# Performance work log

Hardware: AMD Instinct MI355X
Metric: run time of the kernel (lower is better)

## Reference

```python
import jax, jax.numpy as jnp
import numpy as np

N_NODES = 100000
N_EDGES = 1600000
IN_CH = 128
HID = 128
N_GRAPHS = 256


def gcn_conv(x, W, b, src, dst, n_nodes):
    """PyG GCNConv: linear -> symmetric degree normalization with self-loops -> scatter-add -> bias."""
    h = x @ W  # [N, H]
    # degree (in-degree on target index) including the added self-loop
    deg = 1.0 + jax.ops.segment_sum(jnp.ones((dst.shape[0],), x.dtype), dst, num_segments=n_nodes)
    dis = deg ** -0.5  # deg >= 1, no inf guard needed
    coef = dis[src] * dis[dst]  # [E]
    agg = jax.ops.segment_sum(h[src] * coef[:, None], dst, num_segments=n_nodes)
    # self-loop contribution: h[i] * dis[i]^2 = h[i] / deg[i]
    agg = agg + h * (1.0 / deg)[:, None]
    return agg + b


def global_mean_pool(x, batch, n_graphs):
    sums = jax.ops.segment_sum(x, batch, num_segments=n_graphs)
    cnts = jax.ops.segment_sum(jnp.ones((x.shape[0],), x.dtype), batch, num_segments=n_graphs)
    return sums / jnp.maximum(cnts, 1.0)[:, None]


def setup_inputs() -> dict:
    key = jax.random.key(0)
    ks = jax.random.split(key, 8)
    x = jax.random.normal(ks[0], (N_NODES, IN_CH), dtype=jnp.float32)
    edge_index = jax.random.randint(ks[1], (2, N_EDGES), 0, N_NODES, dtype=jnp.int32)
    batch = jnp.sort(jax.random.randint(ks[2], (N_NODES,), 0, N_GRAPHS, dtype=jnp.int32))
    # glorot-ish init for weights
    s1 = (6.0 / (IN_CH + HID)) ** 0.5
    W1 = jax.random.uniform(ks[3], (IN_CH, HID), jnp.float32, -s1, s1)
    b1 = jnp.zeros((HID,), jnp.float32)
    s2 = (6.0 / (HID + HID)) ** 0.5
    W2 = jax.random.uniform(ks[4], (HID, HID), jnp.float32, -s2, s2)
    b2 = jnp.zeros((HID,), jnp.float32)
    s3 = (6.0 / (HID + 1)) ** 0.5
    Wfc = jax.random.uniform(ks[5], (HID, 1), jnp.float32, -s3, s3)
    bfc = jnp.zeros((1,), jnp.float32)
    return {"x": x, "edge_index": edge_index, "batch": batch,
            "W1": W1, "b1": b1, "W2": W2, "b2": b2, "Wfc": Wfc, "bfc": bfc}


def reference(x, edge_index, batch, W1, b1, W2, b2, Wfc, bfc):
    src, dst = edge_index[0], edge_index[1]
    h = jax.nn.relu(gcn_conv(x, W1, b1, src, dst, N_NODES))
    h = jax.nn.relu(gcn_conv(h, W2, b2, src, dst, N_NODES))
    g = global_mean_pool(h, batch, N_GRAPHS)  # [G, H]
    out = g @ Wfc + bfc  # [G, 1]
    return out.squeeze(-1)
```

## Files before the change

kernel.cpp:

```cpp
#include <hip/hip_runtime.h>
#include <hip/hip_bf16.h>

#define N_NODES 100000
#define N_EDGES 1600000
#define HID 128
#define N_GRAPHS 256

#define BSHIFT 9
#define BSIZE 512
#define NBUCK ((N_NODES + BSIZE - 1) / BSIZE)
#define BCAP 12288
#define EPB 8192
#define NBLK_A ((N_EDGES + EPB - 1) / EPB)
#define NCLS 16
#define ZOFF ((uint)N_NODES << 8)

typedef unsigned int uint;
typedef unsigned short ushort;
typedef short short8 __attribute__((ext_vector_type(8)));
typedef float f32x4 __attribute__((ext_vector_type(4)));

__device__ __forceinline__ ushort f2bf_hw(float f) {
    union { __hip_bfloat16 b; ushort u; } cv;
    cv.b = __float2bfloat16(f);
    return cv.u;
}
__device__ __forceinline__ uint4 pack8(const float* r) {
    uint4 o;
    o.x = (uint)f2bf_hw(r[0]) | ((uint)f2bf_hw(r[1]) << 16);
    o.y = (uint)f2bf_hw(r[2]) | ((uint)f2bf_hw(r[3]) << 16);
    o.z = (uint)f2bf_hw(r[4]) | ((uint)f2bf_hw(r[5]) << 16);
    o.w = (uint)f2bf_hw(r[6]) | ((uint)f2bf_hw(r[7]) << 16);
    return o;
}
__device__ __forceinline__ void accp(uint4 v, float2* a) {
    a[0].x += __uint_as_float(v.x << 16);
    a[0].y += __uint_as_float(v.x & 0xFFFF0000u);
    a[1].x += __uint_as_float(v.y << 16);
    a[1].y += __uint_as_float(v.y & 0xFFFF0000u);
    a[2].x += __uint_as_float(v.z << 16);
    a[2].y += __uint_as_float(v.z & 0xFFFF0000u);
    a[3].x += __uint_as_float(v.w << 16);
    a[3].y += __uint_as_float(v.w & 0xFFFF0000u);
}

union Frag16 {
    uint4 u;
    short8 s;
    ushort h[8];
};

__global__ void setup_kernel(int* __restrict__ bfill, int* __restrict__ clshist,
                             int* __restrict__ clsfill,
                             uint4* __restrict__ Azr, uint4* __restrict__ Bzr,
                             const float* __restrict__ W1, const float* __restrict__ W2,
                             uint4* __restrict__ WB1, uint4* __restrict__ WB2) {
    if (blockIdx.x == 0) {
        int t = threadIdx.x;
        if (t < NBUCK) bfill[t] = 0;
        if (t < NCLS) { clshist[t] = 0; clsfill[t] = 0; }
        if (t < 16) Azr[t] = (uint4){0, 0, 0, 0};
        else if (t < 32) Bzr[t - 16] = (uint4){0, 0, 0, 0};
        return;
    }
    int t = (blockIdx.x - 1) * 256 + threadIdx.x;
    const float* W = (t < 2048) ? W1 : W2;
    uint4* WB = (t < 2048) ? WB1 : WB2;
    int tt = t & 2047;
    int lane = tt & 63;
    int nt = (tt >> 6) & 7;
    int kt = tt >> 9;
    int kbase = kt * 32 + (lane >> 4) * 8;
    int col = nt * 16 + (lane & 15);
    float r[8];
#pragma unroll
    for (int j = 0; j < 8; j++) r[j] = W[(size_t)(kbase + j) * 128 + col];
    WB[tt] = pack8(r);
}

__global__ __launch_bounds__(256) void bucket_scatter_kernel(const int* __restrict__ src,
                                                             const int* __restrict__ dst,
                                                             int* __restrict__ bfill,
                                                             uint* __restrict__ bucketed) {
    __shared__ int h[NBUCK];
    __shared__ int rb[NBUCK];
    for (int t = threadIdx.x; t < NBUCK; t += 256) h[t] = 0;
    __syncthreads();
    int base = blockIdx.x * EPB;
#pragma unroll 4
    for (int it = 0; it < EPB / 256; ++it) {
        int e = base + it * 256 + threadIdx.x;
        if (e < N_EDGES) atomicAdd(&h[dst[e] >> BSHIFT], 1);
    }
    __syncthreads();
    for (int t = threadIdx.x; t < NBUCK; t += 256) {
        rb[t] = (h[t] ? atomicAdd(&bfill[t], h[t]) : 0) + t * BCAP;
        h[t] = 0;
    }
    __syncthreads();
#pragma unroll 4
    for (int it = 0; it < EPB / 256; ++it) {
        int e = base + it * 256 + threadIdx.x;
        if (e < N_EDGES) {
            int d = dst[e];
            int b = d >> BSHIFT;
            int pos = rb[b] + atomicAdd(&h[b], 1);
            bucketed[pos] = (uint)src[e] | ((uint)(d & (BSIZE - 1)) << 17);
        }
    }
}

__global__ __launch_bounds__(256) void bucket_csr_kernel(const uint* __restrict__ bucketed,
                                                         const int* __restrict__ bfill,
                                                         int* __restrict__ degi,
                                                         int* __restrict__ rowptr,
                                                         float* __restrict__ dis,
                                                         uint* __restrict__ csrb,
                                                         int* __restrict__ clshist) {
    int b = blockIdx.x;
    int beg = b * BCAP;
    int ne = bfill[b];
    __shared__ int cnt[BSIZE];
    __shared__ int fl[BSIZE];
    __shared__ int ex[BSIZE];
    __shared__ int ps[256];
    __shared__ int ch[NCLS];
    int t = threadIdx.x;
    cnt[t] = 0; cnt[t + 256] = 0;
    fl[t] = 0;  fl[t + 256] = 0;
    if (t < NCLS) ch[t] = 0;
    __syncthreads();
    for (int i = t; i < ne; i += 256) atomicAdd(&cnt[bucketed[beg + i] >> 17], 1);
    __syncthreads();
    int v0 = cnt[2 * t], v1 = cnt[2 * t + 1];
    int p0 = (v0 + 3) & ~3;
    int p1 = (v1 + 3) & ~3;
    int s = p0 + p1;
    ps[t] = s;
    __syncthreads();
    for (int off = 1; off < 256; off <<= 1) {
        int a = (t >= off) ? ps[t - off] : 0;
        __syncthreads();
        ps[t] += a;
        __syncthreads();
    }
    int e0 = ps[t] - s;
    ex[2 * t] = e0;
    ex[2 * t + 1] = e0 + p0;
    int g = b * BSIZE + 2 * t;
    if (g < N_NODES) {
        degi[g] = p0; rowptr[g] = beg + e0;
        dis[g] = rsqrtf(1.0f + (float)v0);
        atomicAdd(&ch[min(p0 >> 2, NCLS - 1)], 1);
    }
    if (g + 1 < N_NODES) {
        degi[g + 1] = p1; rowptr[g + 1] = beg + e0 + p0;
        dis[g + 1] = rsqrtf(1.0f + (float)v1);
        atomicAdd(&ch[min(p1 >> 2, NCLS - 1)], 1);
    }
    __syncthreads();
    if (t < NCLS && ch[t]) atomicAdd(&clshist[t], ch[t]);
    for (int i = t; i < ne; i += 256) {
        uint u = bucketed[beg + i];
        int dl = u >> 17;
        int p = ex[dl] + atomicAdd(&fl[dl], 1);
        csrb[beg + p] = (u & 0x1FFFFu) << 8;
    }
    __syncthreads();
    for (int p = v0; p < p0; ++p) csrb[beg + ex[2 * t] + p] = ZOFF;
    for (int p = v1; p < p1; ++p) csrb[beg + ex[2 * t + 1] + p] = ZOFF;
}

__global__ void clsbase_kernel(const int* __restrict__ clshist, int* __restrict__ clsbase) {
    if (threadIdx.x == 0) {
        int run = 0;
        for (int c = 0; c < NCLS; ++c) { clsbase[c] = run; run += clshist[c]; }
    }
}

__global__ __launch_bounds__(256) void perm_kernel(const int* __restrict__ degi,
                                                   const int* __restrict__ clsbase,
                                                   int* __restrict__ clsfill,
                                                   int* __restrict__ perm) {
    __shared__ int h[NCLS];
    __shared__ int rb[NCLS];
    int t = threadIdx.x;
    if (t < NCLS) h[t] = 0;
    __syncthreads();
    int n = blockIdx.x * 256 + t;
    int cls = 0, myloc = 0;
    if (n < N_NODES) {
        cls = min(degi[n] >> 2, NCLS - 1);
        myloc = atomicAdd(&h[cls], 1);
    }
    __syncthreads();
    if (t < NCLS) rb[t] = h[t] ? (clsbase[t] + atomicAdd(&clsfill[t], h[t])) : 0;
    __syncthreads();
    if (n < N_NODES) perm[rb[cls] + myloc] = n;
}

__global__ __launch_bounds__(256) void xprep_kernel(const float* __restrict__ x,
                                                    const float* __restrict__ dis,
                                                    uint4* __restrict__ Xp) {
    int t = blockIdx.x * 256 + threadIdx.x;
    if (t >= N_NODES * 16) return;
    int n = t >> 4, c16 = t & 15;
    const float* xr = x + (size_t)n * 128 + c16 * 8;
    float d = dis[n];
    float4 lo = *(const float4*)xr;
    float4 hi = *(const float4*)(xr + 4);
    float r[8] = {d * lo.x, d * lo.y, d * lo.z, d * lo.w,
                  d * hi.x, d * hi.y, d * hi.z, d * hi.w};
    Xp[t] = pack8(r);
}

template <int POOL>
__global__ __launch_bounds__(256, 8) void fused_agg_kernel(
    const ushort* __restrict__ T, const uint* __restrict__ csrb,
    const int* __restrict__ rowptr, const int* __restrict__ degi,
    const float* __restrict__ dis, const float* __restrict__ bias,
    const int* __restrict__ perm, const uint4* __restrict__ WB,
    ushort* __restrict__ H, const float* __restrict__ Wfc,
    float* __restrict__ ndot) {
    __shared__ ushort At[16][136];
    __shared__ float disrow[16];
    __shared__ int nid[16];
    __shared__ float pdot[16][4];

    int wave = threadIdx.x >> 6;
    int lane = threadIdx.x & 63;
    int group = lane >> 4;
    int sub = lane & 15;
    uint sub16 = (uint)sub * 16u;
    int r = wave * 4 + group;
    int node = perm[blockIdx.x * 16 + r];
    int start = rowptr[node];
    int iters = degi[node] >> 2;
    const char* Tb = (const char*)T;

    float2 acc[4];
#pragma unroll
    for (int i = 0; i < 4; i++) acc[i] = make_float2(0.f, 0.f);

    int jb = start;
    for (int it = 0; it < iters; ++it, jb += 4) {
        uint o0 = csrb[jb];
        uint o1 = csrb[jb + 1];
        uint o2 = csrb[jb + 2];
        uint o3 = csrb[jb + 3];
        uint4 v0 = *(const uint4*)(Tb + (o0 + sub16));
        uint4 v1 = *(const uint4*)(Tb + (o1 + sub16));
        uint4 v2 = *(const uint4*)(Tb + (o2 + sub16));
        uint4 v3 = *(const uint4*)(Tb + (o3 + sub16));
        accp(v0, acc); accp(v1, acc); accp(v2, acc); accp(v3, acc);
    }
    {
        uint4 sv = *(const uint4*)(Tb + (((uint)node << 8) + sub16));
        accp(sv, acc);
        float di = dis[node];
        float rr[8] = {di * acc[0].x, di * acc[0].y, di * acc[1].x, di * acc[1].y,
                       di * acc[2].x, di * acc[2].y, di * acc[3].x, di * acc[3].y};
        *(uint4*)&At[r][sub * 8] = pack8(rr);
        if (sub == 0) { disrow[r] = di; nid[r] = node; }
    }
    __syncthreads();

    Frag16 a[4];
    int arow = lane & 15;
    int achunk = lane >> 4;
#pragma unroll
    for (int kt = 0; kt < 4; ++kt)
        a[kt].u = *(const uint4*)&At[arow][kt * 32 + achunk * 8];

    f32x4 c0 = (f32x4){0.f, 0.f, 0.f, 0.f};
    f32x4 c1 = (f32x4){0.f, 0.f, 0.f, 0.f};
    int nt0 = wave * 2, nt1 = wave * 2 + 1;
#pragma unroll
    for (int kt = 0; kt < 4; ++kt) {
        Frag16 b0, b1;
        b0.u = WB[(kt * 8 + nt0) * 64 + lane];
        b1.u = WB[(kt * 8 + nt1) * 64 + lane];
        c0 = __builtin_amdgcn_mfma_f32_16x16x32_bf16(a[kt].s, b0.s, c0, 0, 0, 0);
        c1 = __builtin_amdgcn_mfma_f32_16x16x32_bf16(a[kt].s, b1.s, c1, 0, 0, 0);
    }

    int col0 = nt0 * 16 + sub, col1 = nt1 * 16 + sub;
    float b0s = bias[col0], b1s = bias[col1];
    int rq = (lane >> 4) * 4;

    if (POOL == 0) {
        __syncthreads();
#pragma unroll
        for (int reg = 0; reg < 4; ++reg) {
            float sc = disrow[rq + reg];
            At[rq + reg][col0] = f2bf_hw(fmaxf(c0[reg] + b0s, 0.f) * sc);
            At[rq + reg][col1] = f2bf_hw(fmaxf(c1[reg] + b1s, 0.f) * sc);
        }
        __syncthreads();
        int row = threadIdx.x >> 4, c16 = threadIdx.x & 15;
        uint4 v = *(const uint4*)&At[row][c16 * 8];
        *(uint4*)((char*)H + (((size_t)(uint)nid[row]) << 8) + c16 * 16) = v;
    } else {
        float wf0 = Wfc[col0], wf1 = Wfc[col1];
        float p[4];
#pragma unroll
        for (int reg = 0; reg < 4; ++reg)
            p[reg] = fmaxf(c0[reg] + b0s, 0.f) * wf0 + fmaxf(c1[reg] + b1s, 0.f) * wf1;
#pragma unroll
        for (int reg = 0; reg < 4; ++reg) {
            p[reg] += __shfl_xor(p[reg], 1);
            p[reg] += __shfl_xor(p[reg], 2);
            p[reg] += __shfl_xor(p[reg], 4);
            p[reg] += __shfl_xor(p[reg], 8);
        }
        if (sub == 0) {
#pragma unroll
            for (int reg = 0; reg < 4; ++reg) pdot[rq + reg][wave] = p[reg];
        }
        __syncthreads();
        if (threadIdx.x < 16) {
            int row = threadIdx.x;
            ndot[nid[row]] = pdot[row][0] + pdot[row][1] + pdot[row][2] + pdot[row][3];
        }
    }
}

__global__ __launch_bounds__(64) void pool_fc_kernel(const float* __restrict__ ndot,
                                                     const int* __restrict__ batch,
                                                     const float* __restrict__ bfc,
                                                     float* __restrict__ out) {
    int g = blockIdx.x;
    int lane = threadIdx.x;
    auto lb = [&](int key) {
        int lo = 0, hi = N_NODES;
        while (lo < hi) {
            int mid = (lo + hi) >> 1;
            if (batch[mid] < key) lo = mid + 1; else hi = mid;
        }
        return lo;
    };
    int a = lb(g), b = lb(g + 1);
    float s = 0.f;
    for (int i = a + lane; i < b; i += 64) s += ndot[i];
#pragma unroll
    for (int off = 32; off > 0; off >>= 1) s += __shfl_down(s, off);
    if (lane == 0) out[g] = s / fmaxf((float)(b - a), 1.0f) + bfc[0];
}

extern "C" void kernel_launch(void* const* d_in, const int* in_sizes, int n_in,
                              void* d_out, int out_size, void* d_ws, size_t ws_size,
                              hipStream_t stream) {
    const float* x    = (const float*)d_in[0];
    const int*   eidx = (const int*)d_in[1];
    const int*   batch= (const int*)d_in[2];
    const float* W1   = (const float*)d_in[3];
    const float* b1   = (const float*)d_in[4];
    const float* W2   = (const float*)d_in[5];
    const float* b2   = (const float*)d_in[6];
    const float* Wfc  = (const float*)d_in[7];
    const float* bfc  = (const float*)d_in[8];
    float* out = (float*)d_out;

    const int* src = eidx;
    const int* dst = eidx + N_EDGES;

    size_t off = 0;
    char* base = (char*)d_ws;
    auto alloc = [&](size_t bytes) -> void* {
        void* p = base + off;
        off += (bytes + 255) & ~(size_t)255;
        return p;
    };
    int*    bfill   = (int*)alloc(NBUCK * 4);
    int*    clshist = (int*)alloc(NCLS * 4);
    int*    clsfill = (int*)alloc(NCLS * 4);
    int*    clsbase = (int*)alloc(NCLS * 4);
    ushort* A       = (ushort*)alloc((size_t)(N_NODES + 1) * HID * 2);
    ushort* B       = (ushort*)alloc((size_t)(N_NODES + 1) * HID * 2);
    int*    degi    = (int*)alloc(N_NODES * 4);
    int*    rowptr  = (int*)alloc(N_NODES * 4);
    float*  dis     = (float*)alloc(N_NODES * 4);
    float*  ndot    = (float*)alloc(N_NODES * 4);
    int*    perm    = (int*)alloc(N_NODES * 4);
    uint*   csrb    = (uint*)alloc((size_t)NBUCK * BCAP * 4);
    uint*   bucketed= (uint*)alloc((size_t)NBUCK * BCAP * 4);
    uint4*  WB1     = (uint4*)alloc(2048 * 16);
    uint4*  WB2     = (uint4*)alloc(2048 * 16);

    setup_kernel<<<17, 256, 0, stream>>>(bfill, clshist, clsfill,
                                         (uint4*)(A + (size_t)N_NODES * HID),
                                         (uint4*)(B + (size_t)N_NODES * HID),
                                         W1, W2, WB1, WB2);

    bucket_scatter_kernel<<<NBLK_A, 256, 0, stream>>>(src, dst, bfill, bucketed);
    bucket_csr_kernel<<<NBUCK, 256, 0, stream>>>(bucketed, bfill, degi, rowptr, dis,
                                                 csrb, clshist);
    clsbase_kernel<<<1, 64, 0, stream>>>(clshist, clsbase);
    perm_kernel<<<(N_NODES + 255) / 256, 256, 0, stream>>>(degi, clsbase, clsfill, perm);

    xprep_kernel<<<(N_NODES * 16 + 255) / 256, 256, 0, stream>>>(x, dis, (uint4*)A);

    int fgrid = N_NODES / 16;

    fused_agg_kernel<0><<<fgrid, 256, 0, stream>>>(A, csrb, rowptr, degi, dis, b1,
                                                   perm, WB1, B, Wfc, ndot);
    fused_agg_kernel<1><<<fgrid, 256, 0, stream>>>(B, csrb, rowptr, degi, dis, b2,
                                                   perm, WB2, B, Wfc, ndot);

    pool_fc_kernel<<<N_GRAPHS, 64, 0, stream>>>(ndot, batch, bfc, out);
}
```

Measured before the change: 213.2 us.

## Cut kernel launches by merging setup, clsbase, perm and xprep stages

```diff
diff --git a/kernel.cpp b/kernel.cpp
--- a/kernel.cpp
+++ b/kernel.cpp
@@ -50,23 +50,7 @@
     ushort h[8];
 };
 
-__global__ void setup_kernel(int* __restrict__ bfill, int* __restrict__ clshist,
-                             int* __restrict__ clsfill,
-                             uint4* __restrict__ Azr, uint4* __restrict__ Bzr,
-                             const float* __restrict__ W1, const float* __restrict__ W2,
-                             uint4* __restrict__ WB1, uint4* __restrict__ WB2) {
-    if (blockIdx.x == 0) {
-        int t = threadIdx.x;
-        if (t < NBUCK) bfill[t] = 0;
-        if (t < NCLS) { clshist[t] = 0; clsfill[t] = 0; }
-        if (t < 16) Azr[t] = (uint4){0, 0, 0, 0};
-        else if (t < 32) Bzr[t - 16] = (uint4){0, 0, 0, 0};
-        return;
-    }
-    int t = (blockIdx.x - 1) * 256 + threadIdx.x;
-    const float* W = (t < 2048) ? W1 : W2;
-    uint4* WB = (t < 2048) ? WB1 : WB2;
-    int tt = t & 2047;
+__device__ __forceinline__ void pack_w(const float* W, uint4* WB, int tt) {
     int lane = tt & 63;
     int nt = (tt >> 6) & 7;
     int kt = tt >> 9;
@@ -81,7 +65,17 @@
 __global__ __launch_bounds__(256) void bucket_scatter_kernel(const int* __restrict__ src,
                                                              const int* __restrict__ dst,
                                                              int* __restrict__ bfill,
-                                                             uint* __restrict__ bucketed) {
+                                                             uint* __restrict__ bucketed,
+                                                             const float* __restrict__ W1,
+                                                             const float* __restrict__ W2,
+                                                             uint4* __restrict__ WB1,
+                                                             uint4* __restrict__ WB2) {
+    if (blockIdx.x >= NBLK_A) {
+        int t = (blockIdx.x - NBLK_A) * 256 + threadIdx.x;
+        if (t < 2048) pack_w(W1, WB1, t);
+        else          pack_w(W2, WB2, t & 2047);
+        return;
+    }
     __shared__ int h[NBUCK];
     __shared__ int rb[NBUCK];
     for (int t = threadIdx.x; t < NBUCK; t += 256) h[t] = 0;
@@ -116,7 +110,9 @@
                                                          int* __restrict__ rowptr,
                                                          float* __restrict__ dis,
                                                          uint* __restrict__ csrb,
-                                                         int* __restrict__ clshist) {
+                                                         int* __restrict__ clshist,
+                                                         int* __restrict__ donecnt,
+                                                         int* __restrict__ clsbase) {
     int b = blockIdx.x;
     int beg = b * BCAP;
     int ne = bfill[b];
@@ -169,19 +165,27 @@
     __syncthreads();
     for (int p = v0; p < p0; ++p) csrb[beg + ex[2 * t] + p] = ZOFF;
     for (int p = v1; p < p1; ++p) csrb[beg + ex[2 * t + 1] + p] = ZOFF;
-}
-
-__global__ void clsbase_kernel(const int* __restrict__ clshist, int* __restrict__ clsbase) {
-    if (threadIdx.x == 0) {
-        int run = 0;
-        for (int c = 0; c < NCLS; ++c) { clsbase[c] = run; run += clshist[c]; }
-    }
-}
-
-__global__ __launch_bounds__(256) void perm_kernel(const int* __restrict__ degi,
-                                                   const int* __restrict__ clsbase,
-                                                   int* __restrict__ clsfill,
-                                                   int* __restrict__ perm) {
+    __syncthreads();
+    if (t == 0) {
+        __threadfence();
+        int d = atomicAdd(donecnt, 1);
+        if (d == NBUCK - 1) {
+            int run = 0;
+            for (int c = 0; c < NCLS; ++c) {
+                int v = atomicAdd(&clshist[c], 0);
+                clsbase[c] = run; run += v;
+            }
+        }
+    }
+}
+
+__global__ __launch_bounds__(256) void permxprep_kernel(const int* __restrict__ degi,
+                                                        const int* __restrict__ clsbase,
+                                                        int* __restrict__ clsfill,
+                                                        int* __restrict__ perm,
+                                                        const float* __restrict__ x,
+                                                        const float* __restrict__ dis,
+                                                        uint4* __restrict__ Xp) {
     __shared__ int h[NCLS];
     __shared__ int rb[NCLS];
     int t = threadIdx.x;
@@ -197,21 +201,22 @@
     if (t < NCLS) rb[t] = h[t] ? (clsbase[t] + atomicAdd(&clsfill[t], h[t])) : 0;
     __syncthreads();
     if (n < N_NODES) perm[rb[cls] + myloc] = n;
-}
-
-__global__ __launch_bounds__(256) void xprep_kernel(const float* __restrict__ x,
-                                                    const float* __restrict__ dis,
-                                                    uint4* __restrict__ Xp) {
-    int t = blockIdx.x * 256 + threadIdx.x;
-    if (t >= N_NODES * 16) return;
-    int n = t >> 4, c16 = t & 15;
-    const float* xr = x + (size_t)n * 128 + c16 * 8;
-    float d = dis[n];
-    float4 lo = *(const float4*)xr;
-    float4 hi = *(const float4*)(xr + 4);
-    float r[8] = {d * lo.x, d * lo.y, d * lo.z, d * lo.w,
-                  d * hi.x, d * hi.y, d * hi.z, d * hi.w};
-    Xp[t] = pack8(r);
+
+    int base = blockIdx.x * 4096;
+#pragma unroll
+    for (int i = 0; i < 16; ++i) {
+        int idx = base + i * 256 + t;
+        if (idx < N_NODES * 16) {
+            int nn = idx >> 4, c16 = idx & 15;
+            const float* xr = x + (size_t)nn * 128 + c16 * 8;
+            float d = dis[nn];
+            float4 lo = *(const float4*)xr;
+            float4 hi = *(const float4*)(xr + 4);
+            float r[8] = {d * lo.x, d * lo.y, d * lo.z, d * lo.w,
+                          d * hi.x, d * hi.y, d * hi.z, d * hi.w};
+            Xp[idx] = pack8(r);
+        }
+    }
 }
 
 template <int POOL>
@@ -371,9 +376,11 @@
         off += (bytes + 255) & ~(size_t)255;
         return p;
     };
-    int*    bfill   = (int*)alloc(NBUCK * 4);
+    int*    donecnt = (int*)alloc(4);
     int*    clshist = (int*)alloc(NCLS * 4);
     int*    clsfill = (int*)alloc(NCLS * 4);
+    int*    bfill   = (int*)alloc(NBUCK * 4);
+    size_t zero_bytes = off;
     int*    clsbase = (int*)alloc(NCLS * 4);
     ushort* A       = (ushort*)alloc((size_t)(N_NODES + 1) * HID * 2);
     ushort* B       = (ushort*)alloc((size_t)(N_NODES + 1) * HID * 2);
@@ -387,18 +394,16 @@
     uint4*  WB1     = (uint4*)alloc(2048 * 16);
     uint4*  WB2     = (uint4*)alloc(2048 * 16);
 
-    setup_kernel<<<17, 256, 0, stream>>>(bfill, clshist, clsfill,
-                                         (uint4*)(A + (size_t)N_NODES * HID),
-                                         (uint4*)(B + (size_t)N_NODES * HID),
-                                         W1, W2, WB1, WB2);
-
-    bucket_scatter_kernel<<<NBLK_A, 256, 0, stream>>>(src, dst, bfill, bucketed);
+    hipMemsetAsync(base, 0, zero_bytes, stream);
+    hipMemsetAsync(A + (size_t)N_NODES * HID, 0, HID * 2, stream);
+    hipMemsetAsync(B + (size_t)N_NODES * HID, 0, HID * 2, stream);
+
+    bucket_scatter_kernel<<<NBLK_A + 16, 256, 0, stream>>>(src, dst, bfill, bucketed,
+                                                           W1, W2, WB1, WB2);
     bucket_csr_kernel<<<NBUCK, 256, 0, stream>>>(bucketed, bfill, degi, rowptr, dis,
-                                                 csrb, clshist);
-    clsbase_kernel<<<1, 64, 0, stream>>>(clshist, clsbase);
-    perm_kernel<<<(N_NODES + 255) / 256, 256, 0, stream>>>(degi, clsbase, clsfill, perm);
-
-    xprep_kernel<<<(N_NODES * 16 + 255) / 256, 256, 0, stream>>>(x, dis, (uint4*)A);
+                                                 csrb, clshist, donecnt, clsbase);
+    permxprep_kernel<<<(N_NODES + 255) / 256, 256, 0, stream>>>(degi, clsbase, clsfill,
+                                                                perm, x, dis, (uint4*)A);
 
     int fgrid = N_NODES / 16;
 
```

Result: slower. 225.8 us (+5.9%).
